# Optimization experiments

Measured on AMD Instinct MI355X. Metric: run time of the kernel, lower is better.

Reference implementation:

```python
import jax, jax.numpy as jnp
import numpy as np

GROUP_MANTISSA = 8
GROUP_SIZE = 36


def bfp_quantize(x, mantissa=GROUP_MANTISSA, group_size=GROUP_SIZE):
    """Block floating point: flatten, group consecutive group_size elements,
    share the max exponent within each group, keep `mantissa` mantissa bits."""
    flat = x.reshape(-1)
    n = flat.shape[0]
    pad = (-n) % group_size
    f = jnp.pad(flat, (0, pad)).reshape(-1, group_size)  # [G, group_size]
    m = jnp.max(jnp.abs(f), axis=1, keepdims=True)       # group max magnitude
    safe_m = jnp.where(m > 0, m, jnp.ones_like(m))
    e = jnp.floor(jnp.log2(safe_m))                      # shared exponent
    scale = jnp.exp2(e - (mantissa - 1))                 # LSB step for the group
    q = jnp.round(f / scale) * scale
    q = jnp.where(m > 0, q, jnp.zeros_like(q))
    return q.reshape(-1)[:n].reshape(x.shape)


def setup_inputs() -> dict:
    key = jax.random.key(0)
    kx, kw, kb = jax.random.split(key, 3)
    x = jax.random.normal(kx, (32, 64, 112, 112), dtype=jnp.float32)
    # kaiming-uniform-ish scale for a 3x3x64 fan-in
    fan_in = 64 * 3 * 3
    bound = 1.0 / np.sqrt(fan_in)
    weight = jax.random.uniform(kw, (64, 64, 3, 3), dtype=jnp.float32, minval=-bound, maxval=bound) * np.sqrt(3.0)
    bias = jax.random.uniform(kb, (64,), dtype=jnp.float32, minval=-bound, maxval=bound)
    return {"x": x, "weight": weight, "bias": bias}


def reference(x, weight, bias):
    xq = bfp_quantize(x)
    wq = bfp_quantize(weight)
    out = jax.lax.conv_general_dilated(
        xq, wq,
        window_strides=(1, 1),
        padding=((1, 1), (1, 1)),
        lhs_dilation=(1, 1),
        rhs_dilation=(1, 1),
        dimension_numbers=("NCHW", "OIHW", "NCHW"),
        feature_group_count=1,
    )
    return out + bias[None, :, None, None]
```

## Files before the change

kernel.cpp:

```cpp
#include <hip/hip_runtime.h>
#include <hip/hip_bf16.h>

typedef __attribute__((ext_vector_type(4))) float f32x4;
typedef __attribute__((ext_vector_type(8))) short s16x8;

#define X_ELEMS 25690112
#define X_F4    6422528
#define NG_FULL 713614
#define NG      713615
#define HW 112
#define CHW (64*112*112)

__device__ __forceinline__ unsigned short f32_to_bf16_exact(float q) {
    return (unsigned short)(__float_as_uint(q) >> 16);
}

__device__ __forceinline__ void scale_from_max(float m, float& scale, float& inv) {
    if (m > 0.f) {
        int e = (int)((__float_as_uint(m) >> 23) & 0xFF) - 127;
        scale = __builtin_ldexpf(1.0f, e - 7);
        inv   = __builtin_ldexpf(1.0f, 7 - e);
    } else { scale = 0.f; inv = 0.f; }
}

__global__ __launch_bounds__(256) void q1_scales(const float* __restrict__ x,
                                                 float2* __restrict__ sc) {
    __shared__ float lmax[2304];
    int b = blockIdx.x, tid = threadIdx.x;
    long base4 = (long)b * 2304;
    #pragma unroll
    for (int it = 0; it < 9; ++it) {
        int i = it * 256 + tid;
        long g4 = base4 + i;
        float m = 0.f;
        if (g4 < X_F4) {
            float4 v = ((const float4*)x)[g4];
            m = fmaxf(fmaxf(fabsf(v.x), fabsf(v.y)), fmaxf(fabsf(v.z), fabsf(v.w)));
        }
        lmax[i] = m;
    }
    __syncthreads();
    int g = b * 256 + tid;
    if (g < NG) {
        float m = 0.f;
        int o = tid * 9;
        #pragma unroll
        for (int j = 0; j < 9; ++j) m = fmaxf(m, lmax[o + j]);
        float s, inv; scale_from_max(m, s, inv);
        sc[g] = make_float2(s, inv);
    }
}

__global__ __launch_bounds__(256) void qw_kernel(const float* __restrict__ w,
                                                 unsigned short* __restrict__ wt) {
    int g = blockIdx.x * 256 + threadIdx.x;
    if (g >= 1024) return;
    const float4* p = (const float4*)w + g * 9;
    float vv[36]; float m = 0.f;
    #pragma unroll
    for (int i = 0; i < 9; ++i) {
        float4 v = p[i];
        vv[i*4+0]=v.x; vv[i*4+1]=v.y; vv[i*4+2]=v.z; vv[i*4+3]=v.w;
        m = fmaxf(m, fmaxf(fmaxf(fabsf(v.x), fabsf(v.y)), fmaxf(fabsf(v.z), fabsf(v.w))));
    }
    float s, inv; scale_from_max(m, s, inv);
    #pragma unroll
    for (int j = 0; j < 36; ++j) {
        int flat = g * 36 + j;
        int k = flat / 576, rem = flat % 576;
        int c = rem / 9, pp = rem % 9;
        float q = rintf(vv[j] * inv) * s;
        wt[pp * 4096 + k * 64 + c] = f32_to_bf16_exact(q);
    }
}

__global__ __launch_bounds__(256) void q2_quant(const float* __restrict__ x,
                                               const float2* __restrict__ sc,
                                               unsigned short* __restrict__ xt) {
    int n = blockIdx.y, h = blockIdx.x;
    int tid = threadIdx.x;
    int cg = tid >> 7;
    int wv = tid & 127;
    if (wv >= HW) return;
    int base = n * CHW + h * HW + wv;
    int ob = ((n * HW + h) * HW + wv) * 64 + cg * 32;
    #pragma unroll
    for (int jo = 0; jo < 4; ++jo) {
        union { unsigned short u[8]; uint4 d; } pk;
        #pragma unroll
        for (int j = 0; j < 8; ++j) {
            int c = cg * 32 + jo * 8 + j;
            unsigned off = (unsigned)(base + c * 12544);
            float v = x[off];
            float2 s = sc[off / 36u];
            pk.u[j] = f32_to_bf16_exact(rintf(v * s.y) * s.x);
        }
        *(uint4*)(xt + ob + jo * 8) = pk.d;
    }
}

__global__ __launch_bounds__(256, 2) void conv_mfma(const unsigned short* __restrict__ xt,
                                                    const unsigned short* __restrict__ wt,
                                                    const float* __restrict__ bias,
                                                    float* __restrict__ out) {
    __shared__ unsigned short xs[300 * 72];
    const int tid = threadIdx.x;
    const int wave = tid >> 6, lane = tid & 63;
    const int wl = lane & 15, quad = lane >> 4;
    const int kg = wave & 1, mg = wave >> 1;
    const int b = blockIdx.x;
    const int n = b / 56, rem = b % 56;
    const int h0 = (rem >> 2) * 8, w0 = (rem & 3) * 28;

    #pragma unroll
    for (int it = 0; it < 10; ++it) {
        int q = it * 256 + tid;
        if (q < 2400) {
            int pixel = q >> 3, sub = q & 7;
            int r = pixel / 30, col = pixel % 30;
            int hh = h0 + r - 1, ww = w0 + col - 1;
            uint4 v = {0u, 0u, 0u, 0u};
            if (hh >= 0 && hh < HW && ww >= 0 && ww < HW)
                v = *(const uint4*)(xt + (((n * HW + hh) * HW + ww) << 6) + sub * 8);
            *(uint4*)&xs[pixel * 72 + sub * 8] = v;
        }
    }

    s16x8 Bf[9][2][2];
    #pragma unroll
    for (int p = 0; p < 9; ++p)
        #pragma unroll
        for (int cs = 0; cs < 2; ++cs)
            #pragma unroll
            for (int j = 0; j < 2; ++j)
                Bf[p][cs][j] = *(const s16x8*)(wt + p * 4096 +
                                ((kg * 2 + j) * 16 + wl) * 64 + cs * 32 + quad * 8);

    float bv[2];
    #pragma unroll
    for (int j = 0; j < 2; ++j) bv[j] = bias[kg * 32 + j * 16 + wl];

    int pixb[7], eofs[7];
    #pragma unroll
    for (int mti = 0; mti < 7; ++mti) {
        int m = (mg * 7 + mti) * 16 + wl;
        pixb[mti] = (m / 28) * 30 + (m % 28);
        int m0 = (mg * 7 + mti) * 16 + quad * 4;
        eofs[mti] = (m0 / 28) * HW + (m0 % 28);
    }

    __syncthreads();

    f32x4 acc[7][2];
    f32x4 zero = {0.f, 0.f, 0.f, 0.f};
    #pragma unroll
    for (int mti = 0; mti < 7; ++mti) { acc[mti][0] = zero; acc[mti][1] = zero; }

    #pragma unroll
    for (int p = 0; p < 9; ++p) {
        const int dpix = (p / 3) * 30 + (p % 3);
        #pragma unroll
        for (int cs = 0; cs < 2; ++cs) {
            const int cofs = cs * 32 + quad * 8;
            #pragma unroll
            for (int mti = 0; mti < 7; ++mti) {
                s16x8 A = *(const s16x8*)&xs[(pixb[mti] + dpix) * 72 + cofs];
                acc[mti][0] = __builtin_amdgcn_mfma_f32_16x16x32_bf16(A, Bf[p][cs][0], acc[mti][0], 0, 0, 0);
                acc[mti][1] = __builtin_amdgcn_mfma_f32_16x16x32_bf16(A, Bf[p][cs][1], acc[mti][1], 0, 0, 0);
            }
        }
    }

    int obase = n * CHW + h0 * HW + w0;
    #pragma unroll
    for (int mti = 0; mti < 7; ++mti) {
        #pragma unroll
        for (int j = 0; j < 2; ++j) {
            f32x4 v = acc[mti][j];
            v.x += bv[j]; v.y += bv[j]; v.z += bv[j]; v.w += bv[j];
            *(f32x4*)(out + obase + (kg * 32 + j * 16 + wl) * 12544 + eofs[mti]) = v;
        }
    }
}

extern "C" void kernel_launch(void* const* d_in, const int* in_sizes, int n_in,
                              void* d_out, int out_size, void* d_ws, size_t ws_size,
                              hipStream_t stream) {
    const float* x    = (const float*)d_in[0];
    const float* w    = (const float*)d_in[1];
    const float* bias = (const float*)d_in[2];
    float* out = (float*)d_out;
    char* ws = (char*)d_ws;
    unsigned short* xt = (unsigned short*)ws;
    unsigned short* wt = (unsigned short*)(ws + 51380224);
    float2*         sc = (float2*)(ws + 51380224 + 73728);

    hipLaunchKernelGGL(q1_scales, dim3(2788),    dim3(256), 0, stream, x, sc);
    hipLaunchKernelGGL(qw_kernel, dim3(4),       dim3(256), 0, stream, w, wt);
    hipLaunchKernelGGL(q2_quant,  dim3(112, 32), dim3(256), 0, stream, x, sc, xt);
    hipLaunchKernelGGL(conv_mfma, dim3(1792),    dim3(256), 0, stream, xt, wt, bias, out);
}
```

Baseline: 302.5 us.

## Retile conv to 16x16 pixel tiles with channel-octet LDS layout and streamed weights

The conv kernel now uses 16x16 output tiles (1568 blocks) instead of 8x28 strips, stores the haloed input in LDS as channel-octet planes of stride 2600 so that A-fragment reads are contiguous, and streams weight fragments per filter tap with a one-step register prefetch instead of holding all nine taps in registers. This cuts register use so launch bounds can request 3 waves per SIMD. The weight quantization kernel is folded into an extra block of the scale kernel to save a launch. The trade-offs are a larger halo overhead per tile and per-tap global weight loads inside the MFMA loop.

```diff
diff --git a/kernel.cpp b/kernel.cpp
--- a/kernel.cpp
+++ b/kernel.cpp
@@ -10,6 +10,7 @@
 #define NG      713615
 #define HW 112
 #define CHW (64*112*112)
+#define PSTR 2600
 
 __device__ __forceinline__ unsigned short f32_to_bf16_exact(float q) {
     return (unsigned short)(__float_as_uint(q) >> 16);
@@ -24,9 +25,35 @@
 }
 
 __global__ __launch_bounds__(256) void q1_scales(const float* __restrict__ x,
-                                                 float2* __restrict__ sc) {
+                                                 float2* __restrict__ sc,
+                                                 const float* __restrict__ w,
+                                                 unsigned short* __restrict__ wt) {
     __shared__ float lmax[2304];
     int b = blockIdx.x, tid = threadIdx.x;
+    if (b == 2788) {
+        #pragma unroll
+        for (int gi = 0; gi < 4; ++gi) {
+            int g = gi * 256 + tid;
+            const float4* p = (const float4*)w + g * 9;
+            float vv[36]; float m = 0.f;
+            #pragma unroll
+            for (int i = 0; i < 9; ++i) {
+                float4 v = p[i];
+                vv[i*4+0]=v.x; vv[i*4+1]=v.y; vv[i*4+2]=v.z; vv[i*4+3]=v.w;
+                m = fmaxf(m, fmaxf(fmaxf(fabsf(v.x), fabsf(v.y)), fmaxf(fabsf(v.z), fabsf(v.w))));
+            }
+            float s, inv; scale_from_max(m, s, inv);
+            #pragma unroll
+            for (int j = 0; j < 36; ++j) {
+                int flat = g * 36 + j;
+                int k = flat / 576, rem = flat % 576;
+                int c = rem / 9, pp = rem % 9;
+                float q = rintf(vv[j] * inv) * s;
+                wt[pp * 4096 + k * 64 + c] = f32_to_bf16_exact(q);
+            }
+        }
+        return;
+    }
     long base4 = (long)b * 2304;
     #pragma unroll
     for (int it = 0; it < 9; ++it) {
@@ -48,29 +75,6 @@
         for (int j = 0; j < 9; ++j) m = fmaxf(m, lmax[o + j]);
         float s, inv; scale_from_max(m, s, inv);
         sc[g] = make_float2(s, inv);
-    }
-}
-
-__global__ __launch_bounds__(256) void qw_kernel(const float* __restrict__ w,
-                                                 unsigned short* __restrict__ wt) {
-    int g = blockIdx.x * 256 + threadIdx.x;
-    if (g >= 1024) return;
-    const float4* p = (const float4*)w + g * 9;
-    float vv[36]; float m = 0.f;
-    #pragma unroll
-    for (int i = 0; i < 9; ++i) {
-        float4 v = p[i];
-        vv[i*4+0]=v.x; vv[i*4+1]=v.y; vv[i*4+2]=v.z; vv[i*4+3]=v.w;
-        m = fmaxf(m, fmaxf(fmaxf(fabsf(v.x), fabsf(v.y)), fmaxf(fabsf(v.z), fabsf(v.w))));
-    }
-    float s, inv; scale_from_max(m, s, inv);
-    #pragma unroll
-    for (int j = 0; j < 36; ++j) {
-        int flat = g * 36 + j;
-        int k = flat / 576, rem = flat % 576;
-        int c = rem / 9, pp = rem % 9;
-        float q = rintf(vv[j] * inv) * s;
-        wt[pp * 4096 + k * 64 + c] = f32_to_bf16_exact(q);
     }
 }
 
@@ -99,86 +103,92 @@
     }
 }
 
-__global__ __launch_bounds__(256, 2) void conv_mfma(const unsigned short* __restrict__ xt,
+__global__ __launch_bounds__(256, 3) void conv_mfma(const unsigned short* __restrict__ xt,
                                                     const unsigned short* __restrict__ wt,
                                                     const float* __restrict__ bias,
                                                     float* __restrict__ out) {
-    __shared__ unsigned short xs[300 * 72];
+    __shared__ unsigned short xs[8 * PSTR];
     const int tid = threadIdx.x;
     const int wave = tid >> 6, lane = tid & 63;
     const int wl = lane & 15, quad = lane >> 4;
     const int kg = wave & 1, mg = wave >> 1;
     const int b = blockIdx.x;
-    const int n = b / 56, rem = b % 56;
-    const int h0 = (rem >> 2) * 8, w0 = (rem & 3) * 28;
-
-    #pragma unroll
-    for (int it = 0; it < 10; ++it) {
+    const int n = b / 49, rem = b % 49;
+    const int h0 = (rem / 7) * 16, w0 = (rem % 7) * 16;
+
+    s16x8 Bcur[2][2], Bnxt[2][2];
+    #pragma unroll
+    for (int cs = 0; cs < 2; ++cs)
+        #pragma unroll
+        for (int j = 0; j < 2; ++j)
+            Bcur[cs][j] = *(const s16x8*)(wt + (kg * 32 + j * 16 + wl) * 64 + cs * 32 + quad * 8);
+
+    #pragma unroll
+    for (int it = 0; it < 11; ++it) {
         int q = it * 256 + tid;
-        if (q < 2400) {
-            int pixel = q >> 3, sub = q & 7;
-            int r = pixel / 30, col = pixel % 30;
+        if (q < 2592) {
+            int pixel = q >> 3, oct = q & 7;
+            int r = pixel / 18, col = pixel % 18;
             int hh = h0 + r - 1, ww = w0 + col - 1;
             uint4 v = {0u, 0u, 0u, 0u};
             if (hh >= 0 && hh < HW && ww >= 0 && ww < HW)
-                v = *(const uint4*)(xt + (((n * HW + hh) * HW + ww) << 6) + sub * 8);
-            *(uint4*)&xs[pixel * 72 + sub * 8] = v;
-        }
-    }
-
-    s16x8 Bf[9][2][2];
-    #pragma unroll
-    for (int p = 0; p < 9; ++p)
+                v = *(const uint4*)(xt + (((n * HW + hh) * HW + ww) << 6) + oct * 8);
+            *(uint4*)&xs[oct * PSTR + pixel * 8] = v;
+        }
+    }
+
+    float bv[2];
+    #pragma unroll
+    for (int j = 0; j < 2; ++j) bv[j] = bias[kg * 32 + j * 16 + wl];
+
+    int pb[8];
+    #pragma unroll
+    for (int mti = 0; mti < 8; ++mti)
+        pb[mti] = ((mg * 8 + mti) * 18 + wl) * 8;
+
+    f32x4 acc[8][2];
+    f32x4 zero = {0.f, 0.f, 0.f, 0.f};
+    #pragma unroll
+    for (int mti = 0; mti < 8; ++mti) { acc[mti][0] = zero; acc[mti][1] = zero; }
+
+    __syncthreads();
+
+    #pragma unroll
+    for (int p = 0; p < 9; ++p) {
+        if (p < 8) {
+            #pragma unroll
+            for (int cs = 0; cs < 2; ++cs)
+                #pragma unroll
+                for (int j = 0; j < 2; ++j)
+                    Bnxt[cs][j] = *(const s16x8*)(wt + (p + 1) * 4096 +
+                                    (kg * 32 + j * 16 + wl) * 64 + cs * 32 + quad * 8);
+        }
+        const int dpix = ((p / 3) * 18 + (p % 3)) * 8;
+        #pragma unroll
+        for (int cs = 0; cs < 2; ++cs) {
+            const int cbase = (cs * 4 + quad) * PSTR + dpix;
+            #pragma unroll
+            for (int mti = 0; mti < 8; ++mti) {
+                s16x8 A = *(const s16x8*)&xs[cbase + pb[mti]];
+                acc[mti][0] = __builtin_amdgcn_mfma_f32_16x16x32_bf16(A, Bcur[cs][0], acc[mti][0], 0, 0, 0);
+                acc[mti][1] = __builtin_amdgcn_mfma_f32_16x16x32_bf16(A, Bcur[cs][1], acc[mti][1], 0, 0, 0);
+            }
+        }
         #pragma unroll
         for (int cs = 0; cs < 2; ++cs)
             #pragma unroll
             for (int j = 0; j < 2; ++j)
-                Bf[p][cs][j] = *(const s16x8*)(wt + p * 4096 +
-                                ((kg * 2 + j) * 16 + wl) * 64 + cs * 32 + quad * 8);
-
-    float bv[2];
-    #pragma unroll
-    for (int j = 0; j < 2; ++j) bv[j] = bias[kg * 32 + j * 16 + wl];
-
-    int pixb[7], eofs[7];
-    #pragma unroll
-    for (int mti = 0; mti < 7; ++mti) {
-        int m = (mg * 7 + mti) * 16 + wl;
-        pixb[mti] = (m / 28) * 30 + (m % 28);
-        int m0 = (mg * 7 + mti) * 16 + quad * 4;
-        eofs[mti] = (m0 / 28) * HW + (m0 % 28);
-    }
-
-    __syncthreads();
-
-    f32x4 acc[7][2];
-    f32x4 zero = {0.f, 0.f, 0.f, 0.f};
-    #pragma unroll
-    for (int mti = 0; mti < 7; ++mti) { acc[mti][0] = zero; acc[mti][1] = zero; }
-
-    #pragma unroll
-    for (int p = 0; p < 9; ++p) {
-        const int dpix = (p / 3) * 30 + (p % 3);
-        #pragma unroll
-        for (int cs = 0; cs < 2; ++cs) {
-            const int cofs = cs * 32 + quad * 8;
-            #pragma unroll
-            for (int mti = 0; mti < 7; ++mti) {
-                s16x8 A = *(const s16x8*)&xs[(pixb[mti] + dpix) * 72 + cofs];
-                acc[mti][0] = __builtin_amdgcn_mfma_f32_16x16x32_bf16(A, Bf[p][cs][0], acc[mti][0], 0, 0, 0);
-                acc[mti][1] = __builtin_amdgcn_mfma_f32_16x16x32_bf16(A, Bf[p][cs][1], acc[mti][1], 0, 0, 0);
-            }
-        }
-    }
-
-    int obase = n * CHW + h0 * HW + w0;
-    #pragma unroll
-    for (int mti = 0; mti < 7; ++mti) {
+                Bcur[cs][j] = Bnxt[cs][j];
+    }
+
+    int obase = n * CHW + h0 * HW + w0 + quad * 4;
+    #pragma unroll
+    for (int mti = 0; mti < 8; ++mti) {
         #pragma unroll
         for (int j = 0; j < 2; ++j) {
             f32x4 v = acc[mti][j];
             v.x += bv[j]; v.y += bv[j]; v.z += bv[j]; v.w += bv[j];
-            *(f32x4*)(out + obase + (kg * 32 + j * 16 + wl) * 12544 + eofs[mti]) = v;
+            *(f32x4*)(out + obase + (kg * 32 + j * 16 + wl) * 12544 + (mg * 8 + mti) * HW) = v;
         }
     }
 }
@@ -195,8 +205,7 @@
     unsigned short* wt = (unsigned short*)(ws + 51380224);
     float2*         sc = (float2*)(ws + 51380224 + 73728);
 
-    hipLaunchKernelGGL(q1_scales, dim3(2788),    dim3(256), 0, stream, x, sc);
-    hipLaunchKernelGGL(qw_kernel, dim3(4),       dim3(256), 0, stream, w, wt);
+    hipLaunchKernelGGL(q1_scales, dim3(2789),    dim3(256), 0, stream, x, sc, w, wt);
     hipLaunchKernelGGL(q2_quant,  dim3(112, 32), dim3(256), 0, stream, x, sc, xt);
-    hipLaunchKernelGGL(conv_mfma, dim3(1792),    dim3(256), 0, stream, xt, wt, bias, out);
-}
+    hipLaunchKernelGGL(conv_mfma, dim3(1568),    dim3(256), 0, stream, xt, wt, bias, out);
+}
```

New measurement: 361.1 us. 1.19x slower.
